# Performance work log

Measured on AMD Instinct MI355X. Metric: run time of the kernel, lower is better.

The kernel has to match this reference:

```python
import jax, jax.numpy as jnp
import numpy as np

D_MODEL = 1024
N_HEADS = 16
HEAD_DIM = D_MODEL // N_HEADS  # 64
LATENT = 256
B, S = 2, 2048


def setup_inputs() -> dict:
    key = jax.random.key(0)
    ks = jax.random.split(key, 13)
    sc = 0.02
    inp = {
        'x': jax.random.normal(ks[0], (B, S, D_MODEL), jnp.float32),
        'Wq': jax.random.normal(ks[1], (D_MODEL, D_MODEL), jnp.float32) * sc,
        'bq': jnp.zeros((D_MODEL,), jnp.float32),
        'Wkd': jax.random.normal(ks[2], (D_MODEL, LATENT), jnp.float32) * sc,
        'bkd': jnp.zeros((LATENT,), jnp.float32),
        'Wvd': jax.random.normal(ks[3], (D_MODEL, LATENT), jnp.float32) * sc,
        'bvd': jnp.zeros((LATENT,), jnp.float32),
        'Wku': jax.random.normal(ks[4], (LATENT, D_MODEL), jnp.float32) * sc,
        'bku': jnp.zeros((D_MODEL,), jnp.float32),
        'Wvu': jax.random.normal(ks[5], (LATENT, D_MODEL), jnp.float32) * sc,
        'bvu': jnp.zeros((D_MODEL,), jnp.float32),
        'Wo': jax.random.normal(ks[6], (D_MODEL, D_MODEL), jnp.float32) * sc,
        'bo': jnp.zeros((D_MODEL,), jnp.float32),
    }
    return inp


def reference(x, Wq, bq, Wkd, bkd, Wvd, bvd, Wku, bku, Wvu, bvu, Wo, bo):
    b, s, _ = x.shape
    # projections
    Q = x @ Wq + bq                      # [b, s, d_model]
    K_latent = x @ Wkd + bkd             # [b, s, latent]
    V_latent = x @ Wvd + bvd             # [b, s, latent]
    K = K_latent @ Wku + bku             # [b, s, d_model]
    V = V_latent @ Wvu + bvu             # [b, s, d_model]
    # split heads
    Qh = Q.reshape(b, s, N_HEADS, HEAD_DIM)
    Kh = K.reshape(b, s, N_HEADS, HEAD_DIM)
    Vh = V.reshape(b, s, N_HEADS, HEAD_DIM)
    scale = 1.0 / jnp.sqrt(jnp.asarray(HEAD_DIM, x.dtype))
    scores = jnp.einsum('bqhd,bkhd->bhqk', Qh, Kh) * scale  # [b,h,s,s]
    attn = jax.nn.softmax(scores, axis=-1)
    ctx = jnp.einsum('bhqk,bkhd->bqhd', attn, Vh).reshape(b, s, D_MODEL)
    out = ctx @ Wo + bo
    return out
```

## Files before the change

### kernel.cpp

```cpp
#include <hip/hip_runtime.h>
#include <hip/hip_bf16.h>
#include <cstddef>

#define B_SZ 2
#define SEQ  2048
#define DM   1024
#define NH   16
#define HD   64
#define LAT  256
#define MTOT (B_SZ*SEQ)
#define NQKV 1536
#define QSCALE 0.18033688011112042f

typedef short bf16x8 __attribute__((ext_vector_type(8)));
typedef float floatx4 __attribute__((ext_vector_type(4)));
typedef unsigned short u16;

#if __has_builtin(__builtin_amdgcn_exp2f)
#define EXP2(x) __builtin_amdgcn_exp2f(x)
#else
#define EXP2(x) exp2f(x)
#endif

__device__ __forceinline__ u16 f2bf(float f) {
  union { float f; unsigned u; } a; a.f = f;
  unsigned r = a.u + 0x7FFFu + ((a.u >> 16) & 1u);
  return (u16)(r >> 16);
}

__device__ __forceinline__ floatx4 mfma16(bf16x8 a, bf16x8 b, floatx4 c) {
  return __builtin_amdgcn_mfma_f32_16x16x32_bf16(a, b, c, 0, 0, 0);
}

__device__ __forceinline__ void load16(const u16* g, u16* l) {
  __builtin_amdgcn_global_load_lds((const __attribute__((address_space(1))) unsigned*)g,
                                   (__attribute__((address_space(3))) unsigned*)l, 16, 0, 0);
}

__device__ void transpose_tile(const float* __restrict__ W, u16* __restrict__ WT,
                               int K, int N, int k0, int n0, u16 (*t)[65]) {
  const int r = threadIdx.x >> 4;
  const int c4 = (threadIdx.x & 15) * 4;
#pragma unroll
  for (int s = 0; s < 4; s++) {
    int row = s * 16 + r;
    float4 v = *(const float4*)&W[(size_t)(k0 + row) * N + n0 + c4];
    t[row][c4 + 0] = f2bf(v.x); t[row][c4 + 1] = f2bf(v.y);
    t[row][c4 + 2] = f2bf(v.z); t[row][c4 + 3] = f2bf(v.w);
  }
  __syncthreads();
  const int r2 = threadIdx.x >> 2;
  const int c8 = (threadIdx.x & 3) * 16;
  __align__(16) u16 tmp[16];
#pragma unroll
  for (int i = 0; i < 16; i++) tmp[i] = t[c8 + i][r2];
  u16* dst = WT + (size_t)(n0 + r2) * K + k0 + c8;
  *(bf16x8*)dst       = *(const bf16x8*)&tmp[0];
  *(bf16x8*)(dst + 8) = *(const bf16x8*)&tmp[8];
}

__global__ __launch_bounds__(256)
void prep_k(const float* __restrict__ x, u16* __restrict__ xb,
            const float* __restrict__ Wq, const float* __restrict__ Wkd,
            const float* __restrict__ Wvd, const float* __restrict__ Wku,
            const float* __restrict__ Wvu, const float* __restrict__ Wo,
            u16* __restrict__ WstkT, u16* __restrict__ WkuT,
            u16* __restrict__ WvuT, u16* __restrict__ WoT,
            const float* __restrict__ bq, const float* __restrict__ bkd,
            const float* __restrict__ bvd, float* __restrict__ bqkv) {
  __shared__ u16 t[64][65];
  const int blk = blockIdx.x;
  if (blk < 4096) {
    int i = blk * 256 + threadIdx.x;
    float4 v = ((const float4*)x)[i];
    ushort4 o; o.x = f2bf(v.x); o.y = f2bf(v.y); o.z = f2bf(v.z); o.w = f2bf(v.w);
    ((ushort4*)xb)[i] = o;
  } else if (blk < 4352) {
    int tt = blk - 4096;
    transpose_tile(Wq, WstkT, DM, DM, (tt >> 4) * 64, (tt & 15) * 64, t);
  } else if (blk < 4416) {
    int tt = blk - 4352;
    transpose_tile(Wkd, WstkT + (size_t)DM * DM, DM, LAT, (tt >> 2) * 64, (tt & 3) * 64, t);
  } else if (blk < 4480) {
    int tt = blk - 4416;
    transpose_tile(Wvd, WstkT + (size_t)1280 * DM, DM, LAT, (tt >> 2) * 64, (tt & 3) * 64, t);
  } else if (blk < 4544) {
    int tt = blk - 4480;
    transpose_tile(Wku, WkuT, LAT, DM, (tt >> 4) * 64, (tt & 15) * 64, t);
  } else if (blk < 4608) {
    int tt = blk - 4544;
    transpose_tile(Wvu, WvuT, LAT, DM, (tt >> 4) * 64, (tt & 15) * 64, t);
  } else if (blk < 4864) {
    int tt = blk - 4608;
    transpose_tile(Wo, WoT, DM, DM, (tt >> 4) * 64, (tt & 15) * 64, t);
  } else {
    int i = (blk - 4864) * 256 + threadIdx.x;
    float v = (i < 1024) ? bq[i] : (i < 1280) ? bkd[i - 1024] : bvd[i - 1280];
    bqkv[i] = v;
  }
}

template<int OUT_BF16, int VT1>
__global__ __launch_bounds__(256)
void gemm_bt(const u16* __restrict__ A0, const u16* __restrict__ A1,
             const u16* __restrict__ BT0, const u16* __restrict__ BT1,
             const float* __restrict__ bias0, const float* __restrict__ bias1,
             void* __restrict__ C0, void* __restrict__ C1,
             int M, int N, int Kd, int lda, float qscale, int qcols) {
  __shared__ u16 As[2][128 * 64];
  __shared__ u16 Bs[2][128 * 64];
  const u16* A  = blockIdx.z ? A1 : A0;
  const u16* BT = blockIdx.z ? BT1 : BT0;
  const float* bias = blockIdx.z ? bias1 : bias0;
  void* C = blockIdx.z ? C1 : C0;

  const int tid = threadIdx.x;
  const int m0 = blockIdx.y * 128, n0 = blockIdx.x * 128;
  const int wave = tid >> 6, lane = tid & 63;
  const int l15 = lane & 15, quad = lane >> 4;
  const int wm = (wave >> 1) * 64, wn = (wave & 1) * 64;

  floatx4 acc[4][4];
#pragma unroll
  for (int i = 0; i < 4; i++)
#pragma unroll
    for (int j = 0; j < 4; j++) acc[i][j] = (floatx4){0.f, 0.f, 0.f, 0.f};

  const int tr = tid >> 3;
  const int tc8 = (tid & 7) * 8;
  const u16* Ag = A  + (size_t)(m0 + tr) * lda + tc8;
  const u16* Bg = BT + (size_t)(n0 + tr) * Kd + tc8;

#pragma unroll
  for (int s = 0; s < 4; s++) {
    load16(Ag + (size_t)(s * 32) * lda, &As[0][tid * 8 + s * 2048]);
    load16(Bg + (size_t)(s * 32) * Kd,  &Bs[0][tid * 8 + s * 2048]);
  }

  const int NIT = Kd >> 6;
  for (int it = 0; it < NIT; ++it) {
    const int cur = it & 1, nxt = cur ^ 1;
    __syncthreads();
    if (it + 1 < NIT) {
      const int k0 = (it + 1) * 64;
#pragma unroll
      for (int s = 0; s < 4; s++) {
        load16(Ag + (size_t)(s * 32) * lda + k0, &As[nxt][tid * 8 + s * 2048]);
        load16(Bg + (size_t)(s * 32) * Kd  + k0, &Bs[nxt][tid * 8 + s * 2048]);
      }
    }
#pragma unroll
    for (int kk = 0; kk < 2; kk++) {
      bf16x8 af[4], bfr[4];
#pragma unroll
      for (int i = 0; i < 4; i++) {
        af[i]  = *(const bf16x8*)&As[cur][(wm + i * 16 + l15) * 64 + kk * 32 + quad * 8];
        bfr[i] = *(const bf16x8*)&Bs[cur][(wn + i * 16 + l15) * 64 + kk * 32 + quad * 8];
      }
#pragma unroll
      for (int i = 0; i < 4; i++)
#pragma unroll
        for (int j = 0; j < 4; j++)
          acc[i][j] = mfma16(af[i], bfr[j], acc[i][j]);
    }
  }

  if (VT1 && blockIdx.z == 1) {
#pragma unroll
    for (int i = 0; i < 4; i++) {
      int row = m0 + wm + i * 16 + quad * 4;
      int bb = row >> 11, sb = row & 2047;
#pragma unroll
      for (int j = 0; j < 4; j++) {
        int col = n0 + wn + j * 16 + l15;
        float bv = bias[col];
        union { u16 u[4]; uint2 w2; } tv;
#pragma unroll
        for (int r = 0; r < 4; r++) tv.u[r] = f2bf(acc[i][j][r] + bv);
        *(uint2*)((u16*)C + ((size_t)(bb * 16 + (col >> 6)) * 64 + (col & 63)) * SEQ + sb) = tv.w2;
      }
    }
  } else {
#pragma unroll
    for (int i = 0; i < 4; i++) {
      int row = m0 + wm + i * 16 + quad * 4;
#pragma unroll
      for (int j = 0; j < 4; j++) {
        int col = n0 + wn + j * 16 + l15;
        float bv = bias[col];
        float sc = (col < qcols) ? qscale : 1.f;
#pragma unroll
        for (int r = 0; r < 4; r++) {
          float v = (acc[i][j][r] + bv) * sc;
          if (OUT_BF16) ((u16*)C)[(size_t)(row + r) * N + col] = f2bf(v);
          else          ((float*)C)[(size_t)(row + r) * N + col] = v;
        }
      }
    }
  }
}

__global__ __launch_bounds__(256, 2)
void attn_fused(const u16* __restrict__ Q, const u16* __restrict__ K,
                const u16* __restrict__ VT, u16* __restrict__ CTX) {
  __shared__ float Ocmb[64][68];
  __shared__ float Lw[4][64];
  __shared__ u16 Plds[4][64][40];
  const int bh = blockIdx.y, b = bh >> 4, h = bh & 15;
  const int wave = threadIdx.x >> 6, lane = threadIdx.x & 63;
  const int l15 = lane & 15, quad = lane >> 4;
  const int q0 = blockIdx.x * 64;

  bf16x8 qf[4][2];
  {
    const u16* Qp = Q + (size_t)(b * SEQ + q0 + l15) * NQKV + h * HD + quad * 8;
#pragma unroll
    for (int qi = 0; qi < 4; qi++)
#pragma unroll
      for (int h2 = 0; h2 < 2; h2++)
        qf[qi][h2] = *(const bf16x8*)(Qp + (size_t)qi * 16 * NQKV + h2 * 32);
  }
  const u16* Kp = K + (size_t)(b * SEQ) * DM + h * HD + quad * 8;
  const u16* Vp = VT + ((size_t)bh * HD + l15) * SEQ + quad * 8;

  floatx4 o[4][4];
#pragma unroll
  for (int dt = 0; dt < 4; dt++)
#pragma unroll
    for (int qi = 0; qi < 4; qi++) o[dt][qi] = (floatx4){0.f, 0.f, 0.f, 0.f};
  float ls[4] = {0.f, 0.f, 0.f, 0.f};

  const int kb0 = wave * 512;

  bf16x8 kfb[2][2][2], vfb[2][4];
#pragma unroll
  for (int ki = 0; ki < 2; ki++)
#pragma unroll
    for (int h2 = 0; h2 < 2; h2++)
      kfb[0][ki][h2] = *(const bf16x8*)(Kp + (size_t)(kb0 + ki * 16 + l15) * DM + h2 * 32);
#pragma unroll
  for (int dt = 0; dt < 4; dt++)
    vfb[0][dt] = *(const bf16x8*)(Vp + (size_t)(dt * 16) * SEQ + kb0);

#pragma unroll 2
  for (int it = 0; it < 16; ++it) {
    const int cur = it & 1, nxt = cur ^ 1;
    const int kb = kb0 + it * 32;
    if (it < 15) {
      const int kn = kb + 32;
#pragma unroll
      for (int ki = 0; ki < 2; ki++)
#pragma unroll
        for (int h2 = 0; h2 < 2; h2++)
          kfb[nxt][ki][h2] = *(const bf16x8*)(Kp + (size_t)(kn + ki * 16 + l15) * DM + h2 * 32);
#pragma unroll
      for (int dt = 0; dt < 4; dt++)
        vfb[nxt][dt] = *(const bf16x8*)(Vp + (size_t)(dt * 16) * SEQ + kn);
    }
    unsigned pw[4][4];
#pragma unroll
    for (int qi = 0; qi < 4; qi++) {
#pragma unroll
      for (int ki = 0; ki < 2; ki++) {
        floatx4 z = (floatx4){0.f, 0.f, 0.f, 0.f};
        z = mfma16(kfb[cur][ki][0], qf[qi][0], z);
        z = mfma16(kfb[cur][ki][1], qf[qi][1], z);
        float p0 = EXP2(z[0]), p1 = EXP2(z[1]), p2 = EXP2(z[2]), p3 = EXP2(z[3]);
        ls[qi] += (p0 + p1) + (p2 + p3);
        unsigned u0 = __float_as_uint(p0) + 0x8000u;
        unsigned u1 = __float_as_uint(p1) + 0x8000u;
        unsigned u2 = __float_as_uint(p2) + 0x8000u;
        unsigned u3 = __float_as_uint(p3) + 0x8000u;
        pw[qi][ki * 2]     = __builtin_amdgcn_perm(u1, u0, 0x07060302u);
        pw[qi][ki * 2 + 1] = __builtin_amdgcn_perm(u3, u2, 0x07060302u);
      }
    }
#pragma unroll
    for (int qi = 0; qi < 4; qi++) {
      uint2 w0; w0.x = pw[qi][0]; w0.y = pw[qi][1];
      *(uint2*)&Plds[wave][qi * 16 + l15][quad * 4] = w0;
      uint2 w1; w1.x = pw[qi][2]; w1.y = pw[qi][3];
      *(uint2*)&Plds[wave][qi * 16 + l15][16 + quad * 4] = w1;
    }
#pragma unroll
    for (int qi = 0; qi < 4; qi++) {
      bf16x8 pf = *(const bf16x8*)&Plds[wave][qi * 16 + l15][quad * 8];
#pragma unroll
      for (int dt = 0; dt < 4; dt++)
        o[dt][qi] = mfma16(vfb[cur][dt], pf, o[dt][qi]);
    }
  }

#pragma unroll
  for (int qi = 0; qi < 4; qi++) {
    float v = ls[qi];
    v += __shfl_xor(v, 16);
    v += __shfl_xor(v, 32);
    if (quad == 0) Lw[wave][qi * 16 + l15] = v;
  }
  if (wave == 0) {
#pragma unroll
    for (int dt = 0; dt < 4; dt++)
#pragma unroll
      for (int qi = 0; qi < 4; qi++)
        *(floatx4*)&Ocmb[qi * 16 + l15][dt * 16 + quad * 4] = o[dt][qi];
  }
  __syncthreads();
  if (wave == 1) {
#pragma unroll
    for (int dt = 0; dt < 4; dt++)
#pragma unroll
      for (int qi = 0; qi < 4; qi++) {
        floatx4* pp = (floatx4*)&Ocmb[qi * 16 + l15][dt * 16 + quad * 4];
        *pp = *pp + o[dt][qi];
      }
  }
  __syncthreads();
  if (wave == 2) {
#pragma unroll
    for (int dt = 0; dt < 4; dt++)
#pragma unroll
      for (int qi = 0; qi < 4; qi++) {
        floatx4* pp = (floatx4*)&Ocmb[qi * 16 + l15][dt * 16 + quad * 4];
        *pp = *pp + o[dt][qi];
      }
  }
  __syncthreads();
  if (wave == 3) {
#pragma unroll
    for (int qi = 0; qi < 4; qi++) {
      int qq = qi * 16 + l15;
      float lt = Lw[0][qq] + Lw[1][qq] + Lw[2][qq] + Lw[3][qq];
      float inv = 1.f / lt;
      u16* Crow = CTX + (size_t)(b * SEQ + q0 + qq) * DM + h * HD + quad * 4;
#pragma unroll
      for (int dt = 0; dt < 4; dt++) {
        floatx4 ov = o[dt][qi] + *(const floatx4*)&Ocmb[qq][dt * 16 + quad * 4];
        union { u16 u[4]; uint2 w2; } tv;
#pragma unroll
        for (int r = 0; r < 4; r++) tv.u[r] = f2bf(ov[r] * inv);
        *(uint2*)(Crow + dt * 16) = tv.w2;
      }
    }
  }
}

extern "C" void kernel_launch(void* const* d_in, const int* in_sizes, int n_in,
                              void* d_out, int out_size, void* d_ws, size_t ws_size,
                              hipStream_t stream) {
  const float* x   = (const float*)d_in[0];
  const float* Wq  = (const float*)d_in[1];
  const float* bq  = (const float*)d_in[2];
  const float* Wkd = (const float*)d_in[3];
  const float* bkd = (const float*)d_in[4];
  const float* Wvd = (const float*)d_in[5];
  const float* bvd = (const float*)d_in[6];
  const float* Wku = (const float*)d_in[7];
  const float* bku = (const float*)d_in[8];
  const float* Wvu = (const float*)d_in[9];
  const float* bvu = (const float*)d_in[10];
  const float* Wo  = (const float*)d_in[11];
  const float* bo  = (const float*)d_in[12];
  float* out = (float*)d_out;

  float* bqkv = (float*)d_ws;
  u16* p = (u16*)((char*)d_ws + 1536 * sizeof(float));
  u16* xb    = p; p += (size_t)MTOT * DM;
  u16* WstkT = p; p += (size_t)NQKV * DM;
  u16* WkuT  = p; p += (size_t)DM * LAT;
  u16* WvuT  = p; p += (size_t)DM * LAT;
  u16* WoT   = p; p += (size_t)DM * DM;
  u16* QKVb  = p; p += (size_t)MTOT * NQKV;
  u16* Kb    = p; p += (size_t)MTOT * DM;
  u16* VTb   = p; p += (size_t)MTOT * DM;
  u16* CXb   = p; p += (size_t)MTOT * DM;

  prep_k<<<4870, 256, 0, stream>>>(x, xb, Wq, Wkd, Wvd, Wku, Wvu, Wo,
                                   WstkT, WkuT, WvuT, WoT, bq, bkd, bvd, bqkv);

  gemm_bt<1, 0><<<dim3(NQKV / 128, MTOT / 128, 1), 256, 0, stream>>>(
      xb, xb, WstkT, WstkT, bqkv, bqkv, QKVb, QKVb, MTOT, NQKV, DM, DM, QSCALE, DM);
  gemm_bt<1, 1><<<dim3(DM / 128, MTOT / 128, 2), 256, 0, stream>>>(
      QKVb + 1024, QKVb + 1280, WkuT, WvuT, bku, bvu, Kb, VTb, MTOT, DM, LAT, NQKV, 1.f, 0);

  attn_fused<<<dim3(SEQ / 64, B_SZ * NH), 256, 0, stream>>>(QKVb, Kb, VTb, CXb);

  gemm_bt<0, 0><<<dim3(DM / 128, MTOT / 128, 1), 256, 0, stream>>>(
      CXb, CXb, WoT, WoT, bo, bo, out, out, MTOT, DM, DM, DM, 1.f, 0);
}
```

Measured before the change: 230.7 us.

## Fold latent down/up projections into combined K/V weights, single QKV GEMM

Precomputes the combined weights Wkd·Wku and Wvd·Wvu (each 1024x1024) with a small GEMM, plus folded biases, so one x-projection GEMM yields Q, K and V directly. This removes the separate latent-to-full up-projection GEMM and the latent intermediate round trip. The V output is transposed through LDS and written with coalesced 16-byte stores. In exchange the main GEMM grows from K-dim paths of 1024x1536 plus 256x2048 to 1024x3072, raising FLOPs, and the folded bias runs a serial 256-term loop per output inside prep.

```diff
diff --git a/kernel.cpp b/kernel.cpp
--- a/kernel.cpp
+++ b/kernel.cpp
@@ -9,7 +9,7 @@
 #define HD   64
 #define LAT  256
 #define MTOT (B_SZ*SEQ)
-#define NQKV 1536
+#define LDQK 2048
 #define QSCALE 0.18033688011112042f
 
 typedef short bf16x8 __attribute__((ext_vector_type(8)));
@@ -64,10 +64,12 @@
             const float* __restrict__ Wq, const float* __restrict__ Wkd,
             const float* __restrict__ Wvd, const float* __restrict__ Wku,
             const float* __restrict__ Wvu, const float* __restrict__ Wo,
-            u16* __restrict__ WstkT, u16* __restrict__ WkuT,
+            u16* __restrict__ Wbig, u16* __restrict__ WkuT,
             u16* __restrict__ WvuT, u16* __restrict__ WoT,
+            u16* __restrict__ Wkd_b, u16* __restrict__ Wvd_b,
             const float* __restrict__ bq, const float* __restrict__ bkd,
-            const float* __restrict__ bvd, float* __restrict__ bqkv) {
+            const float* __restrict__ bvd, const float* __restrict__ bku,
+            const float* __restrict__ bvu, float* __restrict__ bQKV) {
   __shared__ u16 t[64][65];
   const int blk = blockIdx.x;
   if (blk < 4096) {
@@ -77,38 +79,49 @@
     ((ushort4*)xb)[i] = o;
   } else if (blk < 4352) {
     int tt = blk - 4096;
-    transpose_tile(Wq, WstkT, DM, DM, (tt >> 4) * 64, (tt & 15) * 64, t);
+    transpose_tile(Wq, Wbig, DM, DM, (tt >> 4) * 64, (tt & 15) * 64, t);
   } else if (blk < 4416) {
     int tt = blk - 4352;
-    transpose_tile(Wkd, WstkT + (size_t)DM * DM, DM, LAT, (tt >> 2) * 64, (tt & 3) * 64, t);
+    transpose_tile(Wku, WkuT, LAT, DM, (tt & 3) * 64, (tt >> 2) * 64, t);
   } else if (blk < 4480) {
     int tt = blk - 4416;
-    transpose_tile(Wvd, WstkT + (size_t)1280 * DM, DM, LAT, (tt >> 2) * 64, (tt & 3) * 64, t);
-  } else if (blk < 4544) {
+    transpose_tile(Wvu, WvuT, LAT, DM, (tt & 3) * 64, (tt >> 2) * 64, t);
+  } else if (blk < 4736) {
     int tt = blk - 4480;
-    transpose_tile(Wku, WkuT, LAT, DM, (tt >> 4) * 64, (tt & 15) * 64, t);
-  } else if (blk < 4608) {
-    int tt = blk - 4544;
-    transpose_tile(Wvu, WvuT, LAT, DM, (tt >> 4) * 64, (tt & 15) * 64, t);
-  } else if (blk < 4864) {
-    int tt = blk - 4608;
     transpose_tile(Wo, WoT, DM, DM, (tt >> 4) * 64, (tt & 15) * 64, t);
+  } else if (blk < 4992) {
+    int i = (blk - 4736) * 256 + threadIdx.x;
+    float4 v = ((const float4*)Wkd)[i];
+    ushort4 o; o.x = f2bf(v.x); o.y = f2bf(v.y); o.z = f2bf(v.z); o.w = f2bf(v.w);
+    ((ushort4*)Wkd_b)[i] = o;
+  } else if (blk < 5248) {
+    int i = (blk - 4992) * 256 + threadIdx.x;
+    float4 v = ((const float4*)Wvd)[i];
+    ushort4 o; o.x = f2bf(v.x); o.y = f2bf(v.y); o.z = f2bf(v.z); o.w = f2bf(v.w);
+    ((ushort4*)Wvd_b)[i] = o;
+  } else if (blk < 5252) {
+    int i = (blk - 5248) * 256 + threadIdx.x;
+    bQKV[i] = bq[i];
   } else {
-    int i = (blk - 4864) * 256 + threadIdx.x;
-    float v = (i < 1024) ? bq[i] : (i < 1280) ? bkd[i - 1024] : bvd[i - 1280];
-    bqkv[i] = v;
-  }
-}
-
-template<int OUT_BF16, int VT1>
+    int o = (blk - 5252) * 256 + threadIdx.x;
+    const float* bvec = (o < 1024) ? bkd : bvd;
+    const float* Wup  = (o < 1024) ? Wku : Wvu;
+    const float* badd = (o < 1024) ? bku : bvu;
+    int n = o & 1023;
+    float s = 0.f;
+    for (int c = 0; c < LAT; c++) s += bvec[c] * Wup[(size_t)c * DM + n];
+    bQKV[(o < 1024 ? 1024 : 2048) + n] = s + badd[n];
+  }
+}
+
+template<int OUT_BF16, int VMODE>
 __global__ __launch_bounds__(256)
 void gemm_bt(const u16* __restrict__ A0, const u16* __restrict__ A1,
              const u16* __restrict__ BT0, const u16* __restrict__ BT1,
              const float* __restrict__ bias0, const float* __restrict__ bias1,
-             void* __restrict__ C0, void* __restrict__ C1,
-             int M, int N, int Kd, int lda, float qscale, int qcols) {
-  __shared__ u16 As[2][128 * 64];
-  __shared__ u16 Bs[2][128 * 64];
+             void* __restrict__ C0, void* __restrict__ C1, u16* __restrict__ Cvt,
+             int M, int N, int Kd, int lda, int ldc, float qscale, int qcols) {
+  __shared__ u16 smem[32768];
   const u16* A  = blockIdx.z ? A1 : A0;
   const u16* BT = blockIdx.z ? BT1 : BT0;
   const float* bias = blockIdx.z ? bias1 : bias0;
@@ -133,20 +146,20 @@
 
 #pragma unroll
   for (int s = 0; s < 4; s++) {
-    load16(Ag + (size_t)(s * 32) * lda, &As[0][tid * 8 + s * 2048]);
-    load16(Bg + (size_t)(s * 32) * Kd,  &Bs[0][tid * 8 + s * 2048]);
+    load16(Ag + (size_t)(s * 32) * lda, &smem[tid * 8 + s * 2048]);
+    load16(Bg + (size_t)(s * 32) * Kd,  &smem[16384 + tid * 8 + s * 2048]);
   }
 
   const int NIT = Kd >> 6;
   for (int it = 0; it < NIT; ++it) {
-    const int cur = it & 1, nxt = cur ^ 1;
+    const int cur = (it & 1) * 8192, nxt = cur ^ 8192;
     __syncthreads();
     if (it + 1 < NIT) {
       const int k0 = (it + 1) * 64;
 #pragma unroll
       for (int s = 0; s < 4; s++) {
-        load16(Ag + (size_t)(s * 32) * lda + k0, &As[nxt][tid * 8 + s * 2048]);
-        load16(Bg + (size_t)(s * 32) * Kd  + k0, &Bs[nxt][tid * 8 + s * 2048]);
+        load16(Ag + (size_t)(s * 32) * lda + k0, &smem[nxt + tid * 8 + s * 2048]);
+        load16(Bg + (size_t)(s * 32) * Kd  + k0, &smem[16384 + nxt + tid * 8 + s * 2048]);
       }
     }
 #pragma unroll
@@ -154,8 +167,8 @@
       bf16x8 af[4], bfr[4];
 #pragma unroll
       for (int i = 0; i < 4; i++) {
-        af[i]  = *(const bf16x8*)&As[cur][(wm + i * 16 + l15) * 64 + kk * 32 + quad * 8];
-        bfr[i] = *(const bf16x8*)&Bs[cur][(wn + i * 16 + l15) * 64 + kk * 32 + quad * 8];
+        af[i]  = *(const bf16x8*)&smem[cur + (wm + i * 16 + l15) * 64 + kk * 32 + quad * 8];
+        bfr[i] = *(const bf16x8*)&smem[16384 + cur + (wn + i * 16 + l15) * 64 + kk * 32 + quad * 8];
       }
 #pragma unroll
       for (int i = 0; i < 4; i++)
@@ -165,21 +178,29 @@
     }
   }
 
-  if (VT1 && blockIdx.z == 1) {
+  if (VMODE == 1 && n0 >= 2048) {
+    __syncthreads();
 #pragma unroll
     for (int i = 0; i < 4; i++) {
-      int row = m0 + wm + i * 16 + quad * 4;
-      int bb = row >> 11, sb = row & 2047;
+      int rl = wm + i * 16 + quad * 4;
 #pragma unroll
       for (int j = 0; j < 4; j++) {
-        int col = n0 + wn + j * 16 + l15;
-        float bv = bias[col];
+        int cl = wn + j * 16 + l15;
+        float bv = bias[n0 + cl];
         union { u16 u[4]; uint2 w2; } tv;
 #pragma unroll
         for (int r = 0; r < 4; r++) tv.u[r] = f2bf(acc[i][j][r] + bv);
-        *(uint2*)((u16*)C + ((size_t)(bb * 16 + (col >> 6)) * 64 + (col & 63)) * SEQ + sb) = tv.w2;
-      }
-    }
+        *(uint2*)&smem[cl * 136 + rl] = tv.w2;
+      }
+    }
+    __syncthreads();
+    const int c = tid >> 1, half = tid & 1;
+    const int gcol = n0 - 2048 + c;
+    const int bb = m0 >> 11, s0 = m0 & 2047;
+    u16* dst = Cvt + ((size_t)(bb * 16 + (gcol >> 6)) * 64 + (gcol & 63)) * SEQ + s0 + half * 64;
+    const u16* src = &smem[c * 136 + half * 64];
+#pragma unroll
+    for (int u = 0; u < 8; u++) *(bf16x8*)(dst + u * 8) = *(const bf16x8*)(src + u * 8);
   } else {
 #pragma unroll
     for (int i = 0; i < 4; i++) {
@@ -192,8 +213,8 @@
 #pragma unroll
         for (int r = 0; r < 4; r++) {
           float v = (acc[i][j][r] + bv) * sc;
-          if (OUT_BF16) ((u16*)C)[(size_t)(row + r) * N + col] = f2bf(v);
-          else          ((float*)C)[(size_t)(row + r) * N + col] = v;
+          if (OUT_BF16) ((u16*)C)[(size_t)(row + r) * ldc + col] = f2bf(v);
+          else          ((float*)C)[(size_t)(row + r) * ldc + col] = v;
         }
       }
     }
@@ -201,8 +222,8 @@
 }
 
 __global__ __launch_bounds__(256, 2)
-void attn_fused(const u16* __restrict__ Q, const u16* __restrict__ K,
-                const u16* __restrict__ VT, u16* __restrict__ CTX) {
+void attn_fused(const u16* __restrict__ QK, const u16* __restrict__ VT,
+                u16* __restrict__ CTX) {
   __shared__ float Ocmb[64][68];
   __shared__ float Lw[4][64];
   __shared__ u16 Plds[4][64][40];
@@ -213,14 +234,14 @@
 
   bf16x8 qf[4][2];
   {
-    const u16* Qp = Q + (size_t)(b * SEQ + q0 + l15) * NQKV + h * HD + quad * 8;
+    const u16* Qp = QK + (size_t)(b * SEQ + q0 + l15) * LDQK + h * HD + quad * 8;
 #pragma unroll
     for (int qi = 0; qi < 4; qi++)
 #pragma unroll
       for (int h2 = 0; h2 < 2; h2++)
-        qf[qi][h2] = *(const bf16x8*)(Qp + (size_t)qi * 16 * NQKV + h2 * 32);
-  }
-  const u16* Kp = K + (size_t)(b * SEQ) * DM + h * HD + quad * 8;
+        qf[qi][h2] = *(const bf16x8*)(Qp + (size_t)qi * 16 * LDQK + h2 * 32);
+  }
+  const u16* Kp = QK + (size_t)(b * SEQ) * LDQK + 1024 + h * HD + quad * 8;
   const u16* Vp = VT + ((size_t)bh * HD + l15) * SEQ + quad * 8;
 
   floatx4 o[4][4];
@@ -237,7 +258,7 @@
   for (int ki = 0; ki < 2; ki++)
 #pragma unroll
     for (int h2 = 0; h2 < 2; h2++)
-      kfb[0][ki][h2] = *(const bf16x8*)(Kp + (size_t)(kb0 + ki * 16 + l15) * DM + h2 * 32);
+      kfb[0][ki][h2] = *(const bf16x8*)(Kp + (size_t)(kb0 + ki * 16 + l15) * LDQK + h2 * 32);
 #pragma unroll
   for (int dt = 0; dt < 4; dt++)
     vfb[0][dt] = *(const bf16x8*)(Vp + (size_t)(dt * 16) * SEQ + kb0);
@@ -252,7 +273,7 @@
       for (int ki = 0; ki < 2; ki++)
 #pragma unroll
         for (int h2 = 0; h2 < 2; h2++)
-          kfb[nxt][ki][h2] = *(const bf16x8*)(Kp + (size_t)(kn + ki * 16 + l15) * DM + h2 * 32);
+          kfb[nxt][ki][h2] = *(const bf16x8*)(Kp + (size_t)(kn + ki * 16 + l15) * LDQK + h2 * 32);
 #pragma unroll
       for (int dt = 0; dt < 4; dt++)
         vfb[nxt][dt] = *(const bf16x8*)(Vp + (size_t)(dt * 16) * SEQ + kn);
@@ -363,28 +384,38 @@
   const float* bo  = (const float*)d_in[12];
   float* out = (float*)d_out;
 
-  float* bqkv = (float*)d_ws;
-  u16* p = (u16*)((char*)d_ws + 1536 * sizeof(float));
+  float* bQKV  = (float*)d_ws;
+  float* zerob = bQKV + 3072;
+  u16* p = (u16*)(zerob + 1024);
   u16* xb    = p; p += (size_t)MTOT * DM;
-  u16* WstkT = p; p += (size_t)NQKV * DM;
+  u16* Wbig  = p; p += (size_t)3072 * DM;
   u16* WkuT  = p; p += (size_t)DM * LAT;
   u16* WvuT  = p; p += (size_t)DM * LAT;
   u16* WoT   = p; p += (size_t)DM * DM;
-  u16* QKVb  = p; p += (size_t)MTOT * NQKV;
-  u16* Kb    = p; p += (size_t)MTOT * DM;
+  u16* Wkd_b = p; p += (size_t)DM * LAT;
+  u16* Wvd_b = p; p += (size_t)DM * LAT;
+  u16* QKb   = p; p += (size_t)MTOT * LDQK;
   u16* VTb   = p; p += (size_t)MTOT * DM;
   u16* CXb   = p; p += (size_t)MTOT * DM;
 
-  prep_k<<<4870, 256, 0, stream>>>(x, xb, Wq, Wkd, Wvd, Wku, Wvu, Wo,
-                                   WstkT, WkuT, WvuT, WoT, bq, bkd, bvd, bqkv);
-
-  gemm_bt<1, 0><<<dim3(NQKV / 128, MTOT / 128, 1), 256, 0, stream>>>(
-      xb, xb, WstkT, WstkT, bqkv, bqkv, QKVb, QKVb, MTOT, NQKV, DM, DM, QSCALE, DM);
-  gemm_bt<1, 1><<<dim3(DM / 128, MTOT / 128, 2), 256, 0, stream>>>(
-      QKVb + 1024, QKVb + 1280, WkuT, WvuT, bku, bvu, Kb, VTb, MTOT, DM, LAT, NQKV, 1.f, 0);
-
-  attn_fused<<<dim3(SEQ / 64, B_SZ * NH), 256, 0, stream>>>(QKVb, Kb, VTb, CXb);
-
-  gemm_bt<0, 0><<<dim3(DM / 128, MTOT / 128, 1), 256, 0, stream>>>(
-      CXb, CXb, WoT, WoT, bo, bo, out, out, MTOT, DM, DM, DM, 1.f, 0);
-}
+  hipMemsetAsync(zerob, 0, 1024 * sizeof(float), stream);
+
+  prep_k<<<5260, 256, 0, stream>>>(x, xb, Wq, Wkd, Wvd, Wku, Wvu, Wo,
+                                   Wbig, WkuT, WvuT, WoT, Wkd_b, Wvd_b,
+                                   bq, bkd, bvd, bku, bvu, bQKV);
+
+  gemm_bt<1, 0><<<dim3(8, 8, 2), 256, 0, stream>>>(
+      WkuT, WvuT, Wkd_b, Wvd_b, zerob, zerob,
+      Wbig + (size_t)1024 * DM, Wbig + (size_t)2048 * DM, nullptr,
+      1024, 1024, LAT, LAT, 1024, 1.f, 0);
+
+  gemm_bt<1, 1><<<dim3(24, 32, 1), 256, 0, stream>>>(
+      xb, xb, Wbig, Wbig, bQKV, bQKV, QKb, QKb, VTb,
+      MTOT, 3072, DM, DM, LDQK, QSCALE, 1024);
+
+  attn_fused<<<dim3(SEQ / 64, B_SZ * NH), 256, 0, stream>>>(QKb, VTb, CXb);
+
+  gemm_bt<0, 0><<<dim3(8, 32, 1), 256, 0, stream>>>(
+      CXb, CXb, WoT, WoT, bo, bo, out, out, nullptr,
+      MTOT, DM, DM, DM, DM, 1.f, 0);
+}
```

Measured after the change: 240.2 us. 4.1% more time.
